# Optimization experiments

Measured on AMD Instinct MI355X. Metric: run time of the kernel, lower is better.

## Reference

```python
import jax, jax.numpy as jnp
import numpy as np

T_TRACK = 256   # tracklets per graph
M_DET = 256     # detections per graph
N_NODES = T_TRACK + M_DET
D_IN = 512      # raw node feature dim (stand-in for CNN crop features)
D_EMB = 256     # node embedding dim
SLACK = 0.2
LAM = 5.0
SINK_ITERS = 8


def box_iou(a, b):
    # a, b: [E,4] boxes (x1,y1,x2,y2)
    ix1 = jnp.maximum(a[:, 0], b[:, 0])
    iy1 = jnp.maximum(a[:, 1], b[:, 1])
    ix2 = jnp.minimum(a[:, 2], b[:, 2])
    iy2 = jnp.minimum(a[:, 3], b[:, 3])
    inter = jnp.clip(ix2 - ix1, 0.0) * jnp.clip(iy2 - iy1, 0.0)
    area_a = (a[:, 2] - a[:, 0]) * (a[:, 3] - a[:, 1])
    area_b = (b[:, 2] - b[:, 0]) * (b[:, 3] - b[:, 1])
    return inter / (area_a + area_b - inter + 1e-8)


def mlp2(x, W1, b1, W2, b2):
    return jax.nn.sigmoid(jax.nn.relu(x @ W1 + b1) @ W2 + b2)


def setup_inputs() -> dict:
    key = jax.random.key(0)
    ks = jax.random.split(key, 16)
    x = jax.random.normal(ks[0], (N_NODES, D_IN), jnp.float32)
    coords = jax.random.uniform(ks[1], (N_NODES, 4), jnp.float32)
    # valid boxes: x1<x2, y1<y2
    c = jax.random.uniform(ks[2], (N_NODES, 2), jnp.float32) * 100.0
    wh = jax.random.uniform(ks[3], (N_NODES, 2), jnp.float32) * 20.0 + 1.0
    coords_original = jnp.concatenate([c, c + wh], axis=1)
    # bipartite edges: track i (node i) <-> det j (node T_TRACK+j), both directions;
    # first T*M edges satisfy src < dst (the half kept by the row<col mask)
    src = jnp.repeat(jnp.arange(T_TRACK, dtype=jnp.int32), M_DET)
    dst = jnp.tile(jnp.arange(M_DET, dtype=jnp.int32) + T_TRACK, T_TRACK)
    edge_index = jnp.stack([jnp.concatenate([src, dst]), jnp.concatenate([dst, src])])
    s = 0.05
    p = lambda k, shp: jax.random.normal(k, shp, jnp.float32) * s
    return dict(
        x=x, coords=coords, coords_original=coords_original, edge_index=edge_index,
        W_cnn=p(ks[4], (D_IN, D_EMB)), b_cnn=jnp.zeros((D_EMB,), jnp.float32),
        Wapp1=p(ks[5], (2 * D_EMB, 128)), bapp1=jnp.zeros((128,), jnp.float32),
        Wapp2=p(ks[6], (128, 1)), bapp2=jnp.zeros((1,), jnp.float32),
        Wg1=p(ks[7], (8, 32)), bg1=jnp.zeros((32,), jnp.float32),
        Wg2=p(ks[8], (32, 1)), bg2=jnp.zeros((1,), jnp.float32),
        Wa1=p(ks[9], (2, 8)), ba1=jnp.zeros((8,), jnp.float32),
        Wa2=p(ks[10], (8, 1)), ba2=jnp.zeros((1,), jnp.float32),
        Wo1=p(ks[11], (D_EMB, D_EMB)), Wo2=p(ks[12], (D_EMB, D_EMB)),
        bo=jnp.zeros((D_EMB,), jnp.float32),
        Wf1=p(ks[13], (2, 8)), bf1=jnp.zeros((8,), jnp.float32),
        Wf2=p(ks[14], (8, 1)), bf2=jnp.zeros((1,), jnp.float32),
    )


def reference(x, coords, coords_original, edge_index, W_cnn, b_cnn, Wapp1, bapp1, Wapp2, bapp2, Wg1, bg1, Wg2, bg2, Wa1, ba1, Wa2, ba2, Wo1, Wo2, bo, Wf1, bf1, Wf2, bf2):
    src, dst = edge_index[0], edge_index[1]
    h = jax.nn.relu(x @ W_cnn + b_cnn)                      # [N, D]
    # per-edge appearance / geometry affinities (vectorized over all edges)
    app = mlp2(jnp.concatenate([h[src], h[dst]], 1), Wapp1, bapp1, Wapp2, bapp2)[:, 0]
    geo = mlp2(jnp.concatenate([coords[src], coords[dst]], 1), Wg1, bg1, Wg2, bg2)[:, 0]
    iou = box_iou(coords_original[src], coords_original[dst])
    e = mlp2(jnp.stack([app, geo], -1), Wa1, ba1, Wa2, ba2)[:, 0]   # [E]
    # message passing (optimNet): edge-gated neighbor aggregation
    agg = jax.ops.segment_sum(e[:, None] * h[src], dst, num_segments=N_NODES)
    out = jax.nn.relu(h @ Wo1 + agg @ Wo2 + bo)             # [N, D]
    # directed (src < dst) half of the edges only
    eh = T_TRACK * M_DET
    a, b = out[src[:eh]], out[dst[:eh]]
    na = jnp.maximum(jnp.linalg.norm(a, axis=-1), 1e-6)
    nb = jnp.maximum(jnp.linalg.norm(b, axis=-1), 1e-6)
    cos = jnp.sum(a * b, -1) / (na * nb)
    score = mlp2(jnp.stack([cos, iou[:eh]], -1), Wf1, bf1, Wf2, bf2)[:, 0]
    # assignment matrix with slack row/col, Sinkhorn normalization
    slack_v = jnp.exp(jnp.float32(LAM * SLACK))
    mat = jnp.full((T_TRACK + 1, M_DET + 1), slack_v, jnp.float32)
    mat = mat.at[:T_TRACK, :M_DET].set(jnp.exp(LAM * score).reshape(T_TRACK, M_DET))
    for _ in range(SINK_ITERS):
        mat = mat / jnp.sum(mat, axis=1, keepdims=True)
        mat = mat / jnp.sum(mat, axis=0, keepdims=True)
    return mat[:T_TRACK, :M_DET].reshape(-1)                # [T*M]
```

## Files before the change

kernel.cpp:

```cpp
#include <hip/hip_runtime.h>
#include <math.h>


__device__ __forceinline__ float sigmoidf_(float x) { return 1.0f / (1.0f + expf(-x)); }

typedef _Float16 h2t __attribute__((ext_vector_type(2)));

__device__ __forceinline__ h2t pack2(float x, float y) {
  h2t r; r.x = (_Float16)x; r.y = (_Float16)y; return r;
}
__device__ __forceinline__ float fdot2f(h2t a, h2t b, float c) {
  return __builtin_amdgcn_fdot2(a, b, c, false);
}
template <int CTRL>
__device__ __forceinline__ float dpp_get(float x) {
  return __builtin_bit_cast(
      float, __builtin_amdgcn_mov_dpp(__builtin_bit_cast(int, x), CTRL, 0xF, 0xF, false));
}
template <int IMM>
__device__ __forceinline__ float swz_get(float x) {
  return __builtin_bit_cast(
      float, __builtin_amdgcn_ds_swizzle(__builtin_bit_cast(int, x), IMM));
}
__device__ __forceinline__ float allred16(float x) {
  x += dpp_get<0xB1>(x);
  x += dpp_get<0x4E>(x);
  x += dpp_get<0x141>(x);
  x += dpp_get<0x140>(x);
  return x;
}

__global__ __launch_bounds__(256)
void k1_h(const float* __restrict__ x, const float* __restrict__ Wc,
          const float* __restrict__ bc, float* __restrict__ h) {
  __shared__ __align__(16) float Ast[32][36];
  __shared__ float Bs[32][33];
  const int tx = threadIdx.x & 31, ty = threadIdx.x >> 5;
  const int bm = blockIdx.y * 32, bn = blockIdx.x * 32;
  float acc[4] = {0.f, 0.f, 0.f, 0.f};
  for (int k0 = 0; k0 < 512; k0 += 32) {
#pragma unroll
    for (int i = 0; i < 4; ++i) {
      int idx = (int)threadIdx.x + i * 256, r = idx >> 5, c = idx & 31;
      Ast[c][r] = x[(bm + r) * 512 + k0 + c];
      Bs[r][c] = Wc[(k0 + r) * 256 + bn + c];
    }
    __syncthreads();
#pragma unroll
    for (int kk = 0; kk < 32; ++kk) {
      const float4 a4 = *reinterpret_cast<const float4*>(&Ast[kk][4 * ty]);
      const float bv = Bs[kk][tx];
      acc[0] = fmaf(a4.x, bv, acc[0]);
      acc[1] = fmaf(a4.y, bv, acc[1]);
      acc[2] = fmaf(a4.z, bv, acc[2]);
      acc[3] = fmaf(a4.w, bv, acc[3]);
    }
    __syncthreads();
  }
  const float bias = bc[bn + tx];
#pragma unroll
  for (int i = 0; i < 4; ++i) {
    const float vv = acc[i] + bias;
    h[(bm + 4 * ty + i) * 256 + bn + tx] = vv > 0.f ? vv : 0.f;
  }
}

__global__ __launch_bounds__(256)
void k2_pqg(const float* __restrict__ h, const float* __restrict__ W1,
            const float* __restrict__ b1, const float* __restrict__ Wo2,
            float* __restrict__ PQG) {
  __shared__ __align__(16) float Ast[32][36];
  __shared__ float Bs[32][33];
  const int tx = threadIdx.x & 31, ty = threadIdx.x >> 5;
  const int bm = blockIdx.y * 32, bn = blockIdx.x * 32;
  float acc[4] = {0.f, 0.f, 0.f, 0.f};
  for (int k0 = 0; k0 < 256; k0 += 32) {
#pragma unroll
    for (int i = 0; i < 4; ++i) {
      int idx = (int)threadIdx.x + i * 256, r = idx >> 5, c = idx & 31;
      Ast[c][r] = h[(bm + r) * 256 + k0 + c];
      float bvv;
      if (bn < 128)       bvv = W1[(k0 + r) * 128 + bn + c];
      else if (bn < 256)  bvv = W1[(256 + k0 + r) * 128 + (bn - 128) + c];
      else                bvv = Wo2[(k0 + r) * 256 + (bn - 256) + c];
      Bs[r][c] = bvv;
    }
    __syncthreads();
#pragma unroll
    for (int kk = 0; kk < 32; ++kk) {
      const float4 a4 = *reinterpret_cast<const float4*>(&Ast[kk][4 * ty]);
      const float bv = Bs[kk][tx];
      acc[0] = fmaf(a4.x, bv, acc[0]);
      acc[1] = fmaf(a4.y, bv, acc[1]);
      acc[2] = fmaf(a4.z, bv, acc[2]);
      acc[3] = fmaf(a4.w, bv, acc[3]);
    }
    __syncthreads();
  }
  const float bias = (bn < 128) ? b1[bn + tx] : 0.f;
#pragma unroll
  for (int i = 0; i < 4; ++i)
    PQG[(bm + 4 * ty + i) * 512 + bn + tx] = acc[i] + bias;
}

__global__ __launch_bounds__(256)
void k3_edges(const float* __restrict__ PQG, const float* __restrict__ coords,
              const float* __restrict__ co, const float* __restrict__ Wapp2,
              const float* __restrict__ bapp2, const float* __restrict__ Wg1,
              const float* __restrict__ bg1, const float* __restrict__ Wg2,
              const float* __restrict__ bg2, const float* __restrict__ Wa1,
              const float* __restrict__ ba1, const float* __restrict__ Wa2,
              const float* __restrict__ ba2, float* __restrict__ E1,
              float* __restrict__ E2, float* __restrict__ iou1) {
  __shared__ __align__(16) float sFix[128], sW2[128], sWg1[256], sGfix[32], sWg2[32];
  __shared__ float sWa1[16], sBa1[8], sWa2[8];
  const int tid = threadIdx.x;
  const int half = blockIdx.x >> 8;
  const int fr = blockIdx.x & 255;
  if (tid < 128) {
    sFix[tid] = PQG[fr * 512 + (half ? 128 + tid : tid)];
    sW2[tid] = Wapp2[tid];
  }
  sWg1[tid] = Wg1[tid & 255];
  if (tid < 32) sWg2[tid] = Wg2[tid];
  if (tid < 16) sWa1[tid] = Wa1[tid];
  if (tid < 8) { sBa1[tid] = ba1[tid]; sWa2[tid] = Wa2[tid]; }
  __syncthreads();
  if (tid < 32) {
    const int offf = half ? 4 : 0;
    float g = bg1[tid];
#pragma unroll
    for (int q = 0; q < 4; ++q) g = fmaf(coords[fr * 4 + q], sWg1[(offf + q) * 32 + tid], g);
    sGfix[tid] = g;
  }
  __syncthreads();

  const int d = tid;
  const int pnode = 256 + d;
  const float* tb = PQG + pnode * 512 + (half ? 0 : 128);
  float z = 0.f;
#pragma unroll
  for (int j = 0; j < 128; j += 4) {
    const float4 q4 = *reinterpret_cast<const float4*>(tb + j);
    const float4 pf = *reinterpret_cast<const float4*>(&sFix[j]);
    const float4 w4 = *reinterpret_cast<const float4*>(&sW2[j]);
    float a;
    a = pf.x + q4.x; a = a > 0.f ? a : 0.f; z = fmaf(a, w4.x, z);
    a = pf.y + q4.y; a = a > 0.f ? a : 0.f; z = fmaf(a, w4.y, z);
    a = pf.z + q4.z; a = a > 0.f ? a : 0.f; z = fmaf(a, w4.z, z);
    a = pf.w + q4.w; a = a > 0.f ? a : 0.f; z = fmaf(a, w4.w, z);
  }
  const float app = sigmoidf_(z + bapp2[0]);
  const float4 cp = *reinterpret_cast<const float4*>(coords + pnode * 4);
  const int offp = half ? 0 : 4;
  float gz = 0.f;
#pragma unroll
  for (int mb = 0; mb < 8; ++mb) {
    const float4 g4 = *reinterpret_cast<const float4*>(&sGfix[4 * mb]);
    const float4 w0 = *reinterpret_cast<const float4*>(&sWg1[(offp + 0) * 32 + 4 * mb]);
    const float4 w1 = *reinterpret_cast<const float4*>(&sWg1[(offp + 1) * 32 + 4 * mb]);
    const float4 w2 = *reinterpret_cast<const float4*>(&sWg1[(offp + 2) * 32 + 4 * mb]);
    const float4 w3 = *reinterpret_cast<const float4*>(&sWg1[(offp + 3) * 32 + 4 * mb]);
    const float4 v2 = *reinterpret_cast<const float4*>(&sWg2[4 * mb]);
    float hm;
    hm = g4.x + cp.x * w0.x + cp.y * w1.x + cp.z * w2.x + cp.w * w3.x;
    hm = hm > 0.f ? hm : 0.f; gz = fmaf(hm, v2.x, gz);
    hm = g4.y + cp.x * w0.y + cp.y * w1.y + cp.z * w2.y + cp.w * w3.y;
    hm = hm > 0.f ? hm : 0.f; gz = fmaf(hm, v2.y, gz);
    hm = g4.z + cp.x * w0.z + cp.y * w1.z + cp.z * w2.z + cp.w * w3.z;
    hm = hm > 0.f ? hm : 0.f; gz = fmaf(hm, v2.z, gz);
    hm = g4.w + cp.x * w0.w + cp.y * w1.w + cp.z * w2.w + cp.w * w3.w;
    hm = hm > 0.f ? hm : 0.f; gz = fmaf(hm, v2.w, gz);
  }
  const float geo = sigmoidf_(gz + bg2[0]);
  float ez = 0.f;
#pragma unroll
  for (int m = 0; m < 8; ++m) {
    float hm = fmaf(app, sWa1[m], fmaf(geo, sWa1[8 + m], sBa1[m]));
    hm = hm > 0.f ? hm : 0.f;
    ez = fmaf(hm, sWa2[m], ez);
  }
  const float e = sigmoidf_(ez + ba2[0]);
  if (half == 0) {
    E1[fr * 256 + d] = e;
    const float4 A4 = *reinterpret_cast<const float4*>(co + fr * 4);
    const float4 B4 = *reinterpret_cast<const float4*>(co + pnode * 4);
    const float ix1 = fmaxf(A4.x, B4.x), iy1 = fmaxf(A4.y, B4.y);
    const float ix2 = fminf(A4.z, B4.z), iy2 = fminf(A4.w, B4.w);
    const float inter = fmaxf(ix2 - ix1, 0.f) * fmaxf(iy2 - iy1, 0.f);
    const float areaA = (A4.z - A4.x) * (A4.w - A4.y);
    const float areaB = (B4.z - B4.x) * (B4.w - B4.y);
    iou1[fr * 256 + d] = inter / (areaA + areaB - inter + 1e-8f);
  } else {
    E2[fr * 256 + d] = e;
  }
}

__global__ __launch_bounds__(256)
void k5_out(const float* __restrict__ hgl, const float* __restrict__ E1,
            const float* __restrict__ E2, const float* __restrict__ PQG,
            const float* __restrict__ Wo1, const float* __restrict__ bo,
            float* __restrict__ outm) {
  __shared__ __align__(16) float Ast[32][36];
  __shared__ float Bs[32][33];
  const int tx = threadIdx.x & 31, ty = threadIdx.x >> 5;
  const int bm = blockIdx.y * 32, bn = blockIdx.x * 32;
  float acc[4] = {0.f, 0.f, 0.f, 0.f};
  for (int k0 = 0; k0 < 512; k0 += 32) {
    const int kp = k0 & 255;
#pragma unroll
    for (int i = 0; i < 4; ++i) {
      int idx = (int)threadIdx.x + i * 256, r = idx >> 5, c = idx & 31;
      if (k0 < 256) {
        Ast[c][r] = hgl[(bm + r) * 256 + kp + c];
        Bs[r][c] = Wo1[(kp + r) * 256 + bn + c];
      } else if (bm < 256) {
        Ast[c][r] = E2[(bm + r) * 256 + kp + c];
        Bs[r][c] = PQG[(256 + kp + r) * 512 + 256 + bn + c];
      } else {
        Ast[r][c] = E1[(kp + r) * 256 + (bm - 256) + c];
        Bs[r][c] = PQG[(kp + r) * 512 + 256 + bn + c];
      }
    }
    __syncthreads();
#pragma unroll
    for (int kk = 0; kk < 32; ++kk) {
      const float4 a4 = *reinterpret_cast<const float4*>(&Ast[kk][4 * ty]);
      const float bv = Bs[kk][tx];
      acc[0] = fmaf(a4.x, bv, acc[0]);
      acc[1] = fmaf(a4.y, bv, acc[1]);
      acc[2] = fmaf(a4.z, bv, acc[2]);
      acc[3] = fmaf(a4.w, bv, acc[3]);
    }
    __syncthreads();
  }
  const float bias = bo[bn + tx];
#pragma unroll
  for (int i = 0; i < 4; ++i) {
    const float vv = acc[i] + bias;
    outm[(bm + 4 * ty + i) * 256 + bn + tx] = vv > 0.f ? vv : 0.f;
  }
}

__global__ __launch_bounds__(256)
void k6_score(const float* __restrict__ outm, const float* __restrict__ iou1,
              const float* __restrict__ Wf1, const float* __restrict__ bf1,
              const float* __restrict__ Wf2, const float* __restrict__ bf2,
              float* __restrict__ Mblk) {
  const int tid = threadIdx.x;
  const int s = blockIdx.x;
  __shared__ __align__(16) float so[256];
  so[tid] = outm[s * 256 + tid];
  __syncthreads();
  const float* od = outm + (256 + tid) * 256;
  float dot = 0.f, na2 = 0.f, nb2 = 0.f;
#pragma unroll 8
  for (int j = 0; j < 256; j += 4) {
    const float4 o4 = *reinterpret_cast<const float4*>(od + j);
    const float4 s4 = *reinterpret_cast<const float4*>(&so[j]);
    dot = fmaf(s4.x, o4.x, dot); dot = fmaf(s4.y, o4.y, dot);
    dot = fmaf(s4.z, o4.z, dot); dot = fmaf(s4.w, o4.w, dot);
    na2 = fmaf(s4.x, s4.x, na2); na2 = fmaf(s4.y, s4.y, na2);
    na2 = fmaf(s4.z, s4.z, na2); na2 = fmaf(s4.w, s4.w, na2);
    nb2 = fmaf(o4.x, o4.x, nb2); nb2 = fmaf(o4.y, o4.y, nb2);
    nb2 = fmaf(o4.z, o4.z, nb2); nb2 = fmaf(o4.w, o4.w, nb2);
  }
  const float na = fmaxf(sqrtf(na2), 1e-6f);
  const float nb = fmaxf(sqrtf(nb2), 1e-6f);
  const float cosv = dot / (na * nb);
  const float i1 = iou1[s * 256 + tid];
  float sz = 0.f;
#pragma unroll
  for (int m = 0; m < 8; ++m) {
    float hm = fmaf(cosv, Wf1[m], fmaf(i1, Wf1[8 + m], bf1[m]));
    hm = hm > 0.f ? hm : 0.f;
    sz = fmaf(hm, Wf2[m], sz);
  }
  const float score = sigmoidf_(sz + bf2[0]);
  Mblk[s * 256 + tid] = expf(5.0f * score);
}

__global__ __launch_bounds__(1024)
void k7_sink(const float* __restrict__ Mg, float* __restrict__ outp) {
  __shared__ __align__(16) float su_f[256];
  __shared__ __align__(16) float svs_f[256];
  __shared__ __align__(16) float psum[16][260];
  __shared__ float wsumU[16], wsumV[4];
  const int tid = threadIdx.x, w = tid >> 6, l = tid & 63;
  const float slack = 2.71828182845904523536f;
  const float INV256 = 0.00390625f;
  const int rev = ((l & 1) << 3) | ((l & 2) << 1) | ((l & 4) >> 1) | ((l & 8) >> 3);
  const bool b0 = l & 1, b1 = l & 2, b2 = l & 4, b3 = l & 8;

  h2t mrA[16], mrB[16];
#pragma unroll
  for (int i = 0; i < 16; ++i) {
    const float4 f = *reinterpret_cast<const float4*>(Mg + (w * 16 + i) * 256 + 4 * l);
    mrA[i] = pack2(f.x, f.y);
    mrB[i] = pack2(f.z, f.w);
  }
  if (tid < 256) svs_f[tid] = 256.0f;
  __syncthreads();

  float sv256 = 1.0f;
  for (int it = 0; it < 8; ++it) {
    const float sv_tot =
        (it == 0) ? 257.0f : (wsumV[0] + wsumV[1] + wsumV[2] + wsumV[3] + sv256);
    const float su256 = 1.0f / (slack * sv_tot);
    const float4 va = *reinterpret_cast<const float4*>(&svs_f[4 * l]);
    const h2t sva = pack2(va.x, va.y), svb = pack2(va.z, va.w);
    float p[16];
#pragma unroll
    for (int i = 0; i < 16; ++i) p[i] = fdot2f(mrA[i], sva, fdot2f(mrB[i], svb, 0.0f));
#pragma unroll
    for (int i = 0; i < 8; ++i) {
      const float keep = b0 ? p[i + 8] : p[i], give = b0 ? p[i] : p[i + 8];
      p[i] = keep + dpp_get<0xB1>(give);
    }
#pragma unroll
    for (int i = 0; i < 4; ++i) {
      const float keep = b1 ? p[i + 4] : p[i], give = b1 ? p[i] : p[i + 4];
      p[i] = keep + dpp_get<0x4E>(give);
    }
#pragma unroll
    for (int i = 0; i < 2; ++i) {
      const float keep = b2 ? p[i + 2] : p[i], give = b2 ? p[i] : p[i + 2];
      p[i] = keep + dpp_get<0x141>(give);
    }
    {
      const float keep = b3 ? p[1] : p[0], give = b3 ? p[0] : p[1];
      p[0] = keep + dpp_get<0x140>(give);
    }
    float S = p[0];
    S += swz_get<0x401F>(S);
    S += __shfl_xor(S, 32, 64);
    const float su_val = 1.0f / (S * INV256 + slack * sv256);
    if (l < 16) su_f[w * 16 + rev] = su_val;
    const float wsU = allred16(su_val);
    if (l == 0) wsumU[w] = wsU;
    __syncthreads();
    float su16[16];
#pragma unroll
    for (int k = 0; k < 16; k += 4) {
      const float4 t = *reinterpret_cast<const float4*>(&su_f[w * 16 + k]);
      su16[k] = t.x; su16[k + 1] = t.y; su16[k + 2] = t.z; su16[k + 3] = t.w;
    }
    float pc0 = 0.f, pc1 = 0.f, pc2 = 0.f, pc3 = 0.f;
#pragma unroll
    for (int i = 0; i < 16; ++i) {
      const float ui = su16[i];
      pc0 = fmaf((float)mrA[i].x, ui, pc0);
      pc1 = fmaf((float)mrA[i].y, ui, pc1);
      pc2 = fmaf((float)mrB[i].x, ui, pc2);
      pc3 = fmaf((float)mrB[i].y, ui, pc3);
    }
    float4 pcv; pcv.x = pc0; pcv.y = pc1; pcv.z = pc2; pcv.w = pc3;
    *reinterpret_cast<float4*>(&psum[w][4 * l]) = pcv;
    __syncthreads();
    const float su_tot = wsumU[0] + wsumU[1] + wsumU[2] + wsumU[3] + wsumU[4] +
                         wsumU[5] + wsumU[6] + wsumU[7] + wsumU[8] + wsumU[9] +
                         wsumU[10] + wsumU[11] + wsumU[12] + wsumU[13] +
                         wsumU[14] + wsumU[15] + su256;
    if (tid < 256) {
      float cs = 0.f;
#pragma unroll
      for (int g = 0; g < 16; ++g) cs += psum[g][tid];
      const float sv_val = 1.0f / (cs + slack * su256);
      svs_f[tid] = 256.0f * sv_val;
      float t = allred16(sv_val);
      t += swz_get<0x401F>(t);
      t += __shfl_xor(t, 32, 64);
      if (l == 0) wsumV[w] = t;
    }
    sv256 = 1.0f / (slack * su_tot);
    __syncthreads();
  }
  const float4 sv4 = *reinterpret_cast<const float4*>(&svs_f[4 * l]);
#pragma unroll
  for (int i = 0; i < 16; ++i) {
    const float uo = su_f[w * 16 + i] * INV256;
    float4 o;
    o.x = uo * (float)mrA[i].x * sv4.x;
    o.y = uo * (float)mrA[i].y * sv4.y;
    o.z = uo * (float)mrB[i].x * sv4.z;
    o.w = uo * (float)mrB[i].y * sv4.w;
    *reinterpret_cast<float4*>(outp + (w * 16 + i) * 256 + 4 * l) = o;
  }
}

extern "C" void kernel_launch(void* const* d_in, const int* in_sizes, int n_in,
                              void* d_out, int out_size, void* d_ws, size_t ws_size,
                              hipStream_t stream) {
  (void)in_sizes; (void)n_in; (void)out_size; (void)ws_size;
  const float* x      = (const float*)d_in[0];
  const float* coords = (const float*)d_in[1];
  const float* co     = (const float*)d_in[2];
  const float* Wc    = (const float*)d_in[4];
  const float* bc    = (const float*)d_in[5];
  const float* Wapp1 = (const float*)d_in[6];
  const float* bapp1 = (const float*)d_in[7];
  const float* Wapp2 = (const float*)d_in[8];
  const float* bapp2 = (const float*)d_in[9];
  const float* Wg1   = (const float*)d_in[10];
  const float* bg1   = (const float*)d_in[11];
  const float* Wg2   = (const float*)d_in[12];
  const float* bg2   = (const float*)d_in[13];
  const float* Wa1   = (const float*)d_in[14];
  const float* ba1   = (const float*)d_in[15];
  const float* Wa2   = (const float*)d_in[16];
  const float* ba2   = (const float*)d_in[17];
  const float* Wo1   = (const float*)d_in[18];
  const float* Wo2   = (const float*)d_in[19];
  const float* bo    = (const float*)d_in[20];
  const float* Wf1   = (const float*)d_in[21];
  const float* bf1   = (const float*)d_in[22];
  const float* Wf2   = (const float*)d_in[23];
  const float* bf2   = (const float*)d_in[24];

  float* ws   = (float*)d_ws;
  float* h    = ws + 0;
  float* PQG  = ws + 131072;
  float* E1   = ws + 393216;
  float* E2   = ws + 458752;
  float* iou1 = ws + 524288;
  float* outm = ws + 589824;
  float* Mblk = ws + 720896;

  k1_h<<<dim3(8, 16), 256, 0, stream>>>(x, Wc, bc, h);
  k2_pqg<<<dim3(16, 16), 256, 0, stream>>>(h, Wapp1, bapp1, Wo2, PQG);
  k3_edges<<<512, 256, 0, stream>>>(PQG, coords, co, Wapp2, bapp2, Wg1, bg1, Wg2,
                                    bg2, Wa1, ba1, Wa2, ba2, E1, E2, iou1);
  k5_out<<<dim3(8, 16), 256, 0, stream>>>(h, E1, E2, PQG, Wo1, bo, outm);
  k6_score<<<256, 256, 0, stream>>>(outm, iou1, Wf1, bf1, Wf2, bf2, Mblk);
  k7_sink<<<1, 1024, 0, stream>>>(Mblk, (float*)d_out);
}
```

Baseline: 105.0 us.

## Double-buffer GEMM tiles with register prefetch and drop one Sinkhorn barrier

The three tiled GEMM kernels (k1_h, k2_pqg, k5_out) now use a two-stage software pipeline. The next A tile is prefetched into registers and written to a double-buffered LDS array while the current tile is being computed. B values are loaded straight from global memory into per-thread register arrays, so the shared B tile goes away. This aims to hide global-load latency behind the FMA loop and remove one barrier per k-step, at the cost of more registers. In the Sinkhorn kernel, a block-wide __syncthreads is replaced by an LDS waitcnt, because the su_f data is only read back by the same wavefront that wrote it.

Measured after the change: 96.00 us. -8.6%, faster.

```diff
diff --git a/kernel.cpp b/kernel.cpp
--- a/kernel.cpp
+++ b/kernel.cpp
@@ -33,28 +33,51 @@
 __global__ __launch_bounds__(256)
 void k1_h(const float* __restrict__ x, const float* __restrict__ Wc,
           const float* __restrict__ bc, float* __restrict__ h) {
-  __shared__ __align__(16) float Ast[32][36];
-  __shared__ float Bs[32][33];
-  const int tx = threadIdx.x & 31, ty = threadIdx.x >> 5;
+  __shared__ __align__(16) float Ast[2][32][36];
+  const int tid = threadIdx.x;
+  const int tx = tid & 31, ty = tid >> 5;
+  const int ar = tid >> 3, ac = (tid & 7) * 4;
   const int bm = blockIdx.y * 32, bn = blockIdx.x * 32;
+  const float* __restrict__ Bp = Wc + bn + tx;
+  const float* __restrict__ Ap = x + (bm + ar) * 512 + ac;
+
+  float4 aA, aB;
+  float bA[32], bB[32];
   float acc[4] = {0.f, 0.f, 0.f, 0.f};
-  for (int k0 = 0; k0 < 512; k0 += 32) {
-#pragma unroll
-    for (int i = 0; i < 4; ++i) {
-      int idx = (int)threadIdx.x + i * 256, r = idx >> 5, c = idx & 31;
-      Ast[c][r] = x[(bm + r) * 512 + k0 + c];
-      Bs[r][c] = Wc[(k0 + r) * 256 + bn + c];
-    }
-    __syncthreads();
-#pragma unroll
-    for (int kk = 0; kk < 32; ++kk) {
-      const float4 a4 = *reinterpret_cast<const float4*>(&Ast[kk][4 * ty]);
-      const float bv = Bs[kk][tx];
-      acc[0] = fmaf(a4.x, bv, acc[0]);
-      acc[1] = fmaf(a4.y, bv, acc[1]);
-      acc[2] = fmaf(a4.z, bv, acc[2]);
-      acc[3] = fmaf(a4.w, bv, acc[3]);
-    }
+
+#define K1_LOAD(T, AREG, BARR)                                         \
+  {                                                                    \
+    AREG = *reinterpret_cast<const float4*>(Ap + (T) * 32);            \
+    _Pragma("unroll") for (int kk = 0; kk < 32; ++kk)                  \
+        BARR[kk] = Bp[((T) * 32 + kk) * 256];                          \
+  }
+#define K1_STORE(BUF, AREG)                                            \
+  {                                                                    \
+    Ast[BUF][ac + 0][ar] = AREG.x; Ast[BUF][ac + 1][ar] = AREG.y;      \
+    Ast[BUF][ac + 2][ar] = AREG.z; Ast[BUF][ac + 3][ar] = AREG.w;      \
+  }
+#define K1_COMP(BUF, BARR)                                             \
+  {                                                                    \
+    _Pragma("unroll") for (int kk = 0; kk < 32; ++kk) {                \
+      const float4 a4 =                                                \
+          *reinterpret_cast<const float4*>(&Ast[BUF][kk][4 * ty]);     \
+      const float bv = BARR[kk];                                       \
+      acc[0] = fmaf(a4.x, bv, acc[0]); acc[1] = fmaf(a4.y, bv, acc[1]);\
+      acc[2] = fmaf(a4.z, bv, acc[2]); acc[3] = fmaf(a4.w, bv, acc[3]);\
+    }                                                                  \
+  }
+
+  K1_LOAD(0, aA, bA);
+  K1_STORE(0, aA);
+  __syncthreads();
+  for (int t = 0; t < 16; t += 2) {
+    K1_LOAD(t + 1, aB, bB);
+    K1_COMP(0, bA);
+    K1_STORE(1, aB);
+    __syncthreads();
+    if (t + 2 < 16) { K1_LOAD(t + 2, aA, bA); }
+    K1_COMP(1, bB);
+    if (t + 2 < 16) { K1_STORE(0, aA); }
     __syncthreads();
   }
   const float bias = bc[bn + tx];
@@ -63,44 +86,74 @@
     const float vv = acc[i] + bias;
     h[(bm + 4 * ty + i) * 256 + bn + tx] = vv > 0.f ? vv : 0.f;
   }
+#undef K1_LOAD
+#undef K1_STORE
+#undef K1_COMP
 }
 
 __global__ __launch_bounds__(256)
 void k2_pqg(const float* __restrict__ h, const float* __restrict__ W1,
             const float* __restrict__ b1, const float* __restrict__ Wo2,
             float* __restrict__ PQG) {
-  __shared__ __align__(16) float Ast[32][36];
-  __shared__ float Bs[32][33];
-  const int tx = threadIdx.x & 31, ty = threadIdx.x >> 5;
+  __shared__ __align__(16) float Ast[2][32][36];
+  const int tid = threadIdx.x;
+  const int tx = tid & 31, ty = tid >> 5;
+  const int ar = tid >> 3, ac = (tid & 7) * 4;
   const int bm = blockIdx.y * 32, bn = blockIdx.x * 32;
+  const int col = bn + tx;
+  const float* __restrict__ Bp;
+  int ldb;
+  if (bn < 128)      { Bp = W1 + col; ldb = 128; }
+  else if (bn < 256) { Bp = W1 + 256 * 128 + (col - 128); ldb = 128; }
+  else               { Bp = Wo2 + (col - 256); ldb = 256; }
+  const float* __restrict__ Ap = h + (bm + ar) * 256 + ac;
+
+  float4 aA, aB;
+  float bA[32], bB[32];
   float acc[4] = {0.f, 0.f, 0.f, 0.f};
-  for (int k0 = 0; k0 < 256; k0 += 32) {
-#pragma unroll
-    for (int i = 0; i < 4; ++i) {
-      int idx = (int)threadIdx.x + i * 256, r = idx >> 5, c = idx & 31;
-      Ast[c][r] = h[(bm + r) * 256 + k0 + c];
-      float bvv;
-      if (bn < 128)       bvv = W1[(k0 + r) * 128 + bn + c];
-      else if (bn < 256)  bvv = W1[(256 + k0 + r) * 128 + (bn - 128) + c];
-      else                bvv = Wo2[(k0 + r) * 256 + (bn - 256) + c];
-      Bs[r][c] = bvv;
-    }
-    __syncthreads();
-#pragma unroll
-    for (int kk = 0; kk < 32; ++kk) {
-      const float4 a4 = *reinterpret_cast<const float4*>(&Ast[kk][4 * ty]);
-      const float bv = Bs[kk][tx];
-      acc[0] = fmaf(a4.x, bv, acc[0]);
-      acc[1] = fmaf(a4.y, bv, acc[1]);
-      acc[2] = fmaf(a4.z, bv, acc[2]);
-      acc[3] = fmaf(a4.w, bv, acc[3]);
-    }
-    __syncthreads();
-  }
-  const float bias = (bn < 128) ? b1[bn + tx] : 0.f;
+
+#define K2_LOAD(T, AREG, BARR)                                         \
+  {                                                                    \
+    AREG = *reinterpret_cast<const float4*>(Ap + (T) * 32);            \
+    _Pragma("unroll") for (int kk = 0; kk < 32; ++kk)                  \
+        BARR[kk] = Bp[((T) * 32 + kk) * ldb];                          \
+  }
+#define K2_STORE(BUF, AREG)                                            \
+  {                                                                    \
+    Ast[BUF][ac + 0][ar] = AREG.x; Ast[BUF][ac + 1][ar] = AREG.y;      \
+    Ast[BUF][ac + 2][ar] = AREG.z; Ast[BUF][ac + 3][ar] = AREG.w;      \
+  }
+#define K2_COMP(BUF, BARR)                                             \
+  {                                                                    \
+    _Pragma("unroll") for (int kk = 0; kk < 32; ++kk) {                \
+      const float4 a4 =                                                \
+          *reinterpret_cast<const float4*>(&Ast[BUF][kk][4 * ty]);     \
+      const float bv = BARR[kk];                                       \
+      acc[0] = fmaf(a4.x, bv, acc[0]); acc[1] = fmaf(a4.y, bv, acc[1]);\
+      acc[2] = fmaf(a4.z, bv, acc[2]); acc[3] = fmaf(a4.w, bv, acc[3]);\
+    }                                                                  \
+  }
+
+  K2_LOAD(0, aA, bA);
+  K2_STORE(0, aA);
+  __syncthreads();
+  for (int t = 0; t < 8; t += 2) {
+    K2_LOAD(t + 1, aB, bB);
+    K2_COMP(0, bA);
+    K2_STORE(1, aB);
+    __syncthreads();
+    if (t + 2 < 8) { K2_LOAD(t + 2, aA, bA); }
+    K2_COMP(1, bB);
+    if (t + 2 < 8) { K2_STORE(0, aA); }
+    __syncthreads();
+  }
+  const float bias = (bn < 128) ? b1[col] : 0.f;
 #pragma unroll
   for (int i = 0; i < 4; ++i)
-    PQG[(bm + 4 * ty + i) * 512 + bn + tx] = acc[i] + bias;
+    PQG[(bm + 4 * ty + i) * 512 + col] = acc[i] + bias;
+#undef K2_LOAD
+#undef K2_STORE
+#undef K2_COMP
 }
 
 __global__ __launch_bounds__(256)
@@ -201,45 +254,80 @@
             const float* __restrict__ E2, const float* __restrict__ PQG,
             const float* __restrict__ Wo1, const float* __restrict__ bo,
             float* __restrict__ outm) {
-  __shared__ __align__(16) float Ast[32][36];
-  __shared__ float Bs[32][33];
-  const int tx = threadIdx.x & 31, ty = threadIdx.x >> 5;
+  __shared__ __align__(16) float Ast[2][32][36];
+  const int tid = threadIdx.x;
+  const int tx = tid & 31, ty = tid >> 5;
+  const int ar = tid >> 3, ac = (tid & 7) * 4;
   const int bm = blockIdx.y * 32, bn = blockIdx.x * 32;
+  const int col = bn + tx;
+  const bool detrows = (bm >= 256);
+  const float* __restrict__ Ap1 = hgl + (bm + ar) * 256 + ac;
+  const float* __restrict__ Bp1 = Wo1 + col;
+  const float* __restrict__ Ap2 = detrows
+      ? (E1 + ar * 256 + (bm - 256) + ac)
+      : (E2 + (bm + ar) * 256 + ac);
+  const float* __restrict__ Bp2 = PQG + (detrows ? 0 : 256 * 512) + 256 + col;
+
+  float4 aA, aB;
+  float bA[32], bB[32];
   float acc[4] = {0.f, 0.f, 0.f, 0.f};
-  for (int k0 = 0; k0 < 512; k0 += 32) {
-    const int kp = k0 & 255;
-#pragma unroll
-    for (int i = 0; i < 4; ++i) {
-      int idx = (int)threadIdx.x + i * 256, r = idx >> 5, c = idx & 31;
-      if (k0 < 256) {
-        Ast[c][r] = hgl[(bm + r) * 256 + kp + c];
-        Bs[r][c] = Wo1[(kp + r) * 256 + bn + c];
-      } else if (bm < 256) {
-        Ast[c][r] = E2[(bm + r) * 256 + kp + c];
-        Bs[r][c] = PQG[(256 + kp + r) * 512 + 256 + bn + c];
-      } else {
-        Ast[r][c] = E1[(kp + r) * 256 + (bm - 256) + c];
-        Bs[r][c] = PQG[(kp + r) * 512 + 256 + bn + c];
-      }
-    }
-    __syncthreads();
-#pragma unroll
-    for (int kk = 0; kk < 32; ++kk) {
-      const float4 a4 = *reinterpret_cast<const float4*>(&Ast[kk][4 * ty]);
-      const float bv = Bs[kk][tx];
-      acc[0] = fmaf(a4.x, bv, acc[0]);
-      acc[1] = fmaf(a4.y, bv, acc[1]);
-      acc[2] = fmaf(a4.z, bv, acc[2]);
-      acc[3] = fmaf(a4.w, bv, acc[3]);
-    }
-    __syncthreads();
-  }
-  const float bias = bo[bn + tx];
+
+#define K5_LOAD(T, AREG, BARR)                                          \
+  {                                                                     \
+    if ((T) < 8) {                                                      \
+      AREG = *reinterpret_cast<const float4*>(Ap1 + (T) * 32);          \
+      _Pragma("unroll") for (int kk = 0; kk < 32; ++kk)                 \
+          BARR[kk] = Bp1[((T) * 32 + kk) * 256];                        \
+    } else {                                                            \
+      const int tk = (T) - 8;                                           \
+      AREG = *reinterpret_cast<const float4*>(                          \
+          Ap2 + tk * 32 * (detrows ? 256 : 1));                         \
+      _Pragma("unroll") for (int kk = 0; kk < 32; ++kk)                 \
+          BARR[kk] = Bp2[(tk * 32 + kk) * 512];                         \
+    }                                                                   \
+  }
+#define K5_STORE(T, BUF, AREG)                                          \
+  {                                                                     \
+    if ((T) >= 8 && detrows) {                                          \
+      *reinterpret_cast<float4*>(&Ast[BUF][ar][ac]) = AREG;             \
+    } else {                                                            \
+      Ast[BUF][ac + 0][ar] = AREG.x; Ast[BUF][ac + 1][ar] = AREG.y;     \
+      Ast[BUF][ac + 2][ar] = AREG.z; Ast[BUF][ac + 3][ar] = AREG.w;     \
+    }                                                                   \
+  }
+#define K5_COMP(BUF, BARR)                                              \
+  {                                                                     \
+    _Pragma("unroll") for (int kk = 0; kk < 32; ++kk) {                 \
+      const float4 a4 =                                                 \
+          *reinterpret_cast<const float4*>(&Ast[BUF][kk][4 * ty]);      \
+      const float bv = BARR[kk];                                        \
+      acc[0] = fmaf(a4.x, bv, acc[0]); acc[1] = fmaf(a4.y, bv, acc[1]); \
+      acc[2] = fmaf(a4.z, bv, acc[2]); acc[3] = fmaf(a4.w, bv, acc[3]); \
+    }                                                                   \
+  }
+
+  K5_LOAD(0, aA, bA);
+  K5_STORE(0, 0, aA);
+  __syncthreads();
+  for (int t = 0; t < 16; t += 2) {
+    K5_LOAD(t + 1, aB, bB);
+    K5_COMP(0, bA);
+    K5_STORE(t + 1, 1, aB);
+    __syncthreads();
+    if (t + 2 < 16) { K5_LOAD(t + 2, aA, bA); }
+    K5_COMP(1, bB);
+    if (t + 2 < 16) { K5_STORE(t + 2, 0, aA); }
+    __syncthreads();
+  }
+  const float bias = bo[col];
 #pragma unroll
   for (int i = 0; i < 4; ++i) {
     const float vv = acc[i] + bias;
-    outm[(bm + 4 * ty + i) * 256 + bn + tx] = vv > 0.f ? vv : 0.f;
-  }
+    outm[(bm + 4 * ty + i) * 256 + col] = vv > 0.f ? vv : 0.f;
+  }
+#undef K5_LOAD
+#undef K5_STORE
+#undef K5_COMP
 }
 
 __global__ __launch_bounds__(256)
@@ -338,7 +426,7 @@
     if (l < 16) su_f[w * 16 + rev] = su_val;
     const float wsU = allred16(su_val);
     if (l == 0) wsumU[w] = wsU;
-    __syncthreads();
+    asm volatile("s_waitcnt lgkmcnt(0)" ::: "memory");
     float su16[16];
 #pragma unroll
     for (int k = 0; k < 16; k += 4) {
```
